# Kernel optimization log

Measured on AMD Instinct MI355X. Metric: run time of the kernel, lower is better.

## Reference

```python
import jax, jax.numpy as jnp
import numpy as np

# ---- config (matches init_kwargs + VMamba/MambaIR SS2D defaults) ----
B, LEN, C, H, W = 2, 3, 64, 64, 64
N_STATE = 16           # d_state
D_INNER = 2 * C        # expand=2
DT_RANK = C // 16      # ceil(d_model/16)
K = 4                  # 4 scan directions
EPS = 1e-5


def _ln_last(x, g, b):
    m = x.mean(-1, keepdims=True)
    v = x.var(-1, keepdims=True)
    return (x - m) * jax.lax.rsqrt(v + EPS) * g + b


def _instance_ln(x):
    # kalman.utils.layer_norm: normalize each sample over (C,H,W), no affine
    m = x.mean(axis=(1, 2, 3), keepdims=True)
    v = x.var(axis=(1, 2, 3), keepdims=True)
    return (x - m) * jax.lax.rsqrt(v + EPS)


def _gn(x, g, b):
    # GroupNorm with num_groups=1 on NCHW
    m = x.mean(axis=(1, 2, 3), keepdims=True)
    v = x.var(axis=(1, 2, 3), keepdims=True)
    return (x - m) * jax.lax.rsqrt(v + EPS) * g[None, :, None, None] + b[None, :, None, None]


def _conv2d(x, w, b, groups=1):
    y = jax.lax.conv_general_dilated(x, w, (1, 1), 'SAME',
            dimension_numbers=('NCHW', 'OIHW', 'NCHW'), feature_group_count=groups)
    return y + b[None, :, None, None]


def _selective_scan(xs, dts, Bs, Cs, A, Ds, dt_bias):
    # xs, dts: (Bt,K,D,L); Bs, Cs: (Bt,K,N,L); A: (K,D,N); Ds, dt_bias: (K,D)
    delta = jax.nn.softplus(dts + dt_bias[None, :, :, None])
    u_t = jnp.moveaxis(xs, -1, 0)      # (L,Bt,K,D)
    d_t = jnp.moveaxis(delta, -1, 0)
    B_t = jnp.moveaxis(Bs, -1, 0)      # (L,Bt,K,N)
    C_t = jnp.moveaxis(Cs, -1, 0)
    h0 = jnp.zeros((xs.shape[0], K, xs.shape[2], A.shape[-1]), xs.dtype)

    def step(h, inp):
        u, d, Bv, Cv = inp
        dA = jnp.exp(d[..., None] * A)                                  # (Bt,K,D,N)
        h = dA * h + d[..., None] * Bv[:, :, None, :] * u[..., None]
        y = jnp.einsum('bkdn,bkn->bkd', h, Cv)
        return h, y

    _, ys = jax.lax.scan(step, h0, (u_t, d_t, B_t, C_t))
    ys = jnp.moveaxis(ys, 0, -1)                                        # (Bt,K,D,L)
    return ys + xs * Ds[None, :, :, None]


def _ss2d(x, in_proj_w, dwconv_w, dwconv_b, x_proj_w, dt_proj_w, dt_proj_b,
          A_logs, Ds, out_norm_g, out_norm_b, out_proj_w):
    Bt, Hh, Ww, Cc = x.shape
    L = Hh * Ww
    xz = x @ in_proj_w.T                               # (Bt,H,W,2*Di)
    xx, z = jnp.split(xz, 2, axis=-1)
    xx = jnp.transpose(xx, (0, 3, 1, 2))               # (Bt,Di,H,W)
    xx = jax.nn.silu(_conv2d(xx, dwconv_w, dwconv_b, groups=D_INNER))
    hw = xx.reshape(Bt, D_INNER, L)
    wh = jnp.transpose(xx, (0, 1, 3, 2)).reshape(Bt, D_INNER, L)
    xs = jnp.stack([hw, wh, hw[..., ::-1], wh[..., ::-1]], axis=1)      # (Bt,4,Di,L)
    x_dbl = jnp.einsum('bkdl,kcd->bkcl', xs, x_proj_w)
    dts = jnp.einsum('bkrl,kdr->bkdl', x_dbl[:, :, :DT_RANK], dt_proj_w)
    Bs = x_dbl[:, :, DT_RANK:DT_RANK + N_STATE]
    Cs = x_dbl[:, :, DT_RANK + N_STATE:]
    A = -jnp.exp(A_logs)                               # (K,Di,N)
    out_y = _selective_scan(xs, dts, Bs, Cs, A, Ds, dt_proj_b)
    inv = out_y[:, 2:4, :, ::-1]

    def wh2hw(y):
        return jnp.transpose(y.reshape(Bt, D_INNER, Ww, Hh), (0, 1, 3, 2)).reshape(Bt, D_INNER, L)

    y = out_y[:, 0] + inv[:, 0] + wh2hw(out_y[:, 1]) + wh2hw(inv[:, 1])
    y = jnp.transpose(y.reshape(Bt, D_INNER, Hh, Ww), (0, 2, 3, 1))
    y = _ln_last(y, out_norm_g, out_norm_b)
    y = y * jax.nn.silu(z)
    return y @ out_proj_w.T


def setup_inputs() -> dict:
    key = jax.random.key(0)
    ks = jax.random.split(key, 16)
    rn = lambda k, s, sc=0.05: jax.random.normal(k, s, jnp.float32) * sc
    inp = {}
    inp['image_sequence'] = jax.random.normal(ks[0], (B, LEN, C, H, W), jnp.float32)
    inp['difficult_zone'] = jax.random.normal(ks[1], (B, C, H, W), jnp.float32)
    inp['sigma'] = jax.random.uniform(ks[2], (B, C, H, W), jnp.float32)
    inp['gn1_g'] = jnp.ones((3 * C,)); inp['gn1_b'] = jnp.zeros((3 * C,))
    inp['conv1_w'] = rn(ks[3], (C, 3 * C, 3, 3)); inp['conv1_b'] = jnp.zeros((C,))
    inp['gn2_g'] = jnp.ones((C,)); inp['gn2_b'] = jnp.zeros((C,))
    inp['conv2_w'] = rn(ks[4], (C, C, 3, 3)); inp['conv2_b'] = jnp.zeros((C,))
    inp['skip_w'] = rn(ks[5], (C, 3 * C, 1, 1)); inp['skip_b'] = jnp.zeros((C,))
    inp['ln1_g'] = jnp.ones((C,)); inp['ln1_b'] = jnp.zeros((C,))
    inp['ln2_g'] = jnp.ones((C,)); inp['ln2_b'] = jnp.zeros((C,))
    inp['in_proj_w'] = rn(ks[6], (2 * D_INNER, C))
    inp['dwconv_w'] = rn(ks[7], (D_INNER, 1, 3, 3)); inp['dwconv_b'] = jnp.zeros((D_INNER,))
    inp['x_proj_w'] = rn(ks[8], (K, DT_RANK + 2 * N_STATE, D_INNER))
    inp['dt_proj_w'] = rn(ks[9], (K, D_INNER, DT_RANK), 0.2)
    inp['dt_proj_b'] = rn(ks[10], (K, D_INNER), 0.1)
    inp['A_logs'] = jnp.log(jnp.broadcast_to(jnp.arange(1, N_STATE + 1, dtype=jnp.float32), (K, D_INNER, N_STATE)))
    inp['Ds'] = jnp.ones((K, D_INNER))
    inp['out_norm_g'] = jnp.ones((D_INNER,)); inp['out_norm_b'] = jnp.zeros((D_INNER,))
    inp['out_proj_w'] = rn(ks[11], (C, D_INNER))
    inp['fc1_w'] = rn(ks[12], (C, C)); inp['fc1_b'] = jnp.zeros((C,))
    inp['fc2_w'] = rn(ks[13], (C, C)); inp['fc2_b'] = jnp.zeros((C,))
    return inp


def reference(image_sequence, difficult_zone, sigma,
              gn1_g, gn1_b, conv1_w, conv1_b, gn2_g, gn2_b, conv2_w, conv2_b, skip_w, skip_b,
              ln1_g, ln1_b, ln2_g, ln2_b,
              in_proj_w, dwconv_w, dwconv_b, x_proj_w, dt_proj_w, dt_proj_b,
              A_logs, Ds, out_norm_g, out_norm_b, out_proj_w,
              fc1_w, fc1_b, fc2_w, fc2_b):
    Bsz, Lf, Cc, Hh, Ww = image_sequence.shape
    # per-frame layer_norm; frames are independent so fold them into batch
    img = _instance_ln(image_sequence.reshape(Bsz * Lf, Cc, Hh, Ww)).reshape(Bsz, Lf, Cc, Hh, Ww)
    dz = jnp.broadcast_to(difficult_zone[:, None], (Bsz, Lf, Cc, Hh, Ww))
    sg = jnp.broadcast_to(sigma[:, None], (Bsz, Lf, Cc, Hh, Ww))
    x = jnp.concatenate([dz, img, sg], axis=2).reshape(Bsz * Lf, 3 * Cc, Hh, Ww)
    # ConvolutionalResBlock (GN -> SiLU -> conv, x2, + 1x1 skip)
    h = _conv2d(jax.nn.silu(_gn(x, gn1_g, gn1_b)), conv1_w, conv1_b)
    h = _conv2d(jax.nn.silu(_gn(h, gn2_g, gn2_b)), conv2_w, conv2_b)
    x = h + _conv2d(x, skip_w, skip_b)
    # VSSBlock (pre-norm): x + SS2D(LN(x)); x + Mlp(LN(x))
    x = jnp.transpose(x, (0, 2, 3, 1))                 # NHWC
    x = x + _ss2d(_ln_last(x, ln1_g, ln1_b), in_proj_w, dwconv_w, dwconv_b,
                  x_proj_w, dt_proj_w, dt_proj_b, A_logs, Ds,
                  out_norm_g, out_norm_b, out_proj_w)
    xm = _ln_last(x, ln2_g, ln2_b)
    x = x + (jax.nn.gelu(xm @ fc1_w.T + fc1_b) @ fc2_w.T + fc2_b)
    x = jnp.transpose(x, (0, 3, 1, 2)).reshape(Bsz, Lf, Cc, Hh, Ww)
    return x
```

## Files before the change

kernel.cpp:

```cpp
#include <hip/hip_runtime.h>
#include <hip/hip_bf16.h>

typedef unsigned short ushortT;
typedef short short8v __attribute__((ext_vector_type(8)));
typedef short short4v __attribute__((ext_vector_type(4)));
typedef float float4v __attribute__((ext_vector_type(4)));

#define NBL 6
#define NC 64
#define NC3 192
#define NHW 4096
#define NK 4
#define NL 4096
#define NCH 128
#define SCLEN 32
#define NSTATE 49152
#define NSAMP 262144

static const size_t F_XCAT  = 0;
static const size_t F_ACT1  = 4718592;
static const size_t F_H1    = 9437184;
static const size_t F_ACT2  = 11010048;
static const size_t F_H2    = 12582912;
static const size_t F_XRES  = 14155776;
static const size_t F_XXIN  = 15728640;
static const size_t F_Z     = 18874368;
static const size_t F_XXC   = 22020096;
static const size_t F_XDBL  = 25165824;
static const size_t F_YS    = 28704768;
static const size_t F_WTS   = 41287680;
static const size_t F_X1    = 44433408;
static const size_t F_X2    = 46006272;
static const size_t F_STATS = 47579136;
static const size_t F_TOTAL = 47579184;

__device__ __forceinline__ float wred64(float v) {
#pragma unroll
  for (int m = 32; m; m >>= 1) v += __shfl_xor(v, m, 64);
  return v;
}

__device__ __forceinline__ float silu(float v) {
  return v / (1.f + __expf(-v));
}

__device__ __forceinline__ ushortT f2bf(float f) {
  unsigned int u = __builtin_bit_cast(unsigned int, f);
  unsigned int r = (u + 0x7FFFu + ((u >> 16) & 1u)) >> 16;
  return (ushortT)r;
}

__device__ __forceinline__ float bf2f(ushortT u) {
  return __builtin_bit_cast(float, (unsigned int)u << 16);
}

__device__ __forceinline__ int map_pos(int k, int l) {
  if (k == 0) return l;
  if (k == 1) return ((l & 63) << 6) | (l >> 6);
  if (k == 2) return 4095 - l;
  int lp = 4095 - l;
  return ((lp & 63) << 6) | (lp >> 6);
}

__device__ __forceinline__ float softplus_fast(float a) {
  float t = exp2f(a * 1.44269504f);
  float r = 0.69314718f * __log2f(1.f + t);
  return (a > 20.f) ? a : r;
}

__device__ __forceinline__ void pow_tree(float E1, float4v& e0, float4v& e1,
                                         float4v& e2, float4v& e3) {
  float E2 = E1 * E1, E3 = E2 * E1, E4 = E2 * E2;
  float E5 = E4 * E1, E6 = E4 * E2, E7 = E4 * E3, E8 = E4 * E4;
  e0[0] = E1; e0[1] = E2; e0[2] = E3; e0[3] = E4;
  e1[0] = E5; e1[1] = E6; e1[2] = E7; e1[3] = E8;
  e2[0] = E8 * E1; e2[1] = E8 * E2; e2[2] = E8 * E3; e2[3] = E8 * E4;
  e3[0] = E8 * E5; e3[1] = E8 * E6; e3[2] = E8 * E7; e3[3] = E8 * E8;
}

__global__ __launch_bounds__(256) void prep_kernel(const float* __restrict__ skw,
                                                   const float* __restrict__ ipw,
                                                   const float* __restrict__ opw,
                                                   const float* __restrict__ f1w,
                                                   const float* __restrict__ f2w,
                                                   const float* __restrict__ c1w,
                                                   const float* __restrict__ c2w,
                                                   const float* __restrict__ Alog,
                                                   float* __restrict__ wt_sk,
                                                   float* __restrict__ wt_ip,
                                                   float* __restrict__ wt_op,
                                                   float* __restrict__ wt_f1,
                                                   float* __restrict__ wt_f2,
                                                   ushortT* __restrict__ wb1,
                                                   ushortT* __restrict__ wb2,
                                                   float* __restrict__ aParam) {
  int bi = blockIdx.x;
  int t = threadIdx.x;
  if (bi < 48) {
    int id = bi * 256 + t;
    int c = id / 64, o = id % 64;
    wt_sk[id] = skw[o * 192 + c];
  } else if (bi < 112) {
    int id = (bi - 48) * 256 + t;
    int c = id / 256, o = id % 256;
    wt_ip[id] = ipw[o * 64 + c];
  } else if (bi < 144) {
    int id = (bi - 112) * 256 + t;
    int c = id / 64, o = id % 64;
    wt_op[id] = opw[o * 128 + c];
  } else if (bi < 160) {
    int id = (bi - 144) * 256 + t;
    int c = id / 64, o = id % 64;
    wt_f1[id] = f1w[o * 64 + c];
  } else if (bi < 176) {
    int id = (bi - 160) * 256 + t;
    int c = id / 64, o = id % 64;
    wt_f2[id] = f2w[o * 64 + c];
  } else if (bi < 608) {
    int id = (bi - 176) * 256 + t;
    int j = id & 7, lane = (id >> 3) & 63, nt = (id >> 9) & 3;
    int rest = id >> 11;
    int kt = rest % 6, tap = rest / 6;
    int oc = nt * 16 + (lane & 15);
    int ic = kt * 32 + ((lane >> 4) << 3) + j;
    int r = tap / 3, s = tap % 3;
    wb1[id] = f2bf(c1w[(((size_t)oc * 192 + ic) * 3 + r) * 3 + s]);
  } else if (bi < 752) {
    int id = (bi - 608) * 256 + t;
    int j = id & 7, lane = (id >> 3) & 63, nt = (id >> 9) & 3;
    int rest = id >> 11;
    int kt = rest % 2, tap = rest / 2;
    int oc = nt * 16 + (lane & 15);
    int ic = kt * 32 + ((lane >> 4) << 3) + j;
    int r = tap / 3, s = tap % 3;
    wb2[id] = f2bf(c2w[(((size_t)oc * 64 + ic) * 3 + r) * 3 + s]);
  } else {
    int kd = (bi - 752) * 256 + t;
    const float* ar = Alog + (size_t)kd * 16;
    float a1v = -__expf(ar[0]) * 1.44269504f;
    bool geom = true;
#pragma unroll
    for (int n = 1; n < 16; ++n) {
      float an = -__expf(ar[n]) * 1.44269504f;
      geom = geom && (fabsf(an - (float)(n + 1) * a1v) <= 1e-3f * fabsf((float)(n + 1) * a1v) + 1e-6f);
    }
    aParam[kd] = a1v;
    aParam[512 + kd] = geom ? 1.f : 0.f;
  }
}

__global__ __launch_bounds__(256) void stats1_all_kernel(const float* __restrict__ img,
                                                         const float* __restrict__ dz,
                                                         const float* __restrict__ sg,
                                                         double* __restrict__ part) {
  int bi = blockIdx.x;
  int s = bi >> 5, j = bi & 31;
  const float* srcb = (s < 6) ? (img + (size_t)s * NSAMP)
                   : (s < 8) ? (dz + (size_t)(s - 6) * NSAMP)
                             : (sg + (size_t)(s - 8) * NSAMP);
  int slice = NSAMP >> 5;
  const float4* p = (const float4*)(srcb + (size_t)j * slice);
  int n4 = slice >> 2;
  double dsum = 0.0, dsq = 0.0;
  for (int i = threadIdx.x; i < n4; i += 256) {
    float4 v = p[i];
    dsum += (double)((v.x + v.y) + (v.z + v.w));
    dsq += (double)v.x * v.x + (double)v.y * v.y + (double)v.z * v.z + (double)v.w * v.w;
  }
  __shared__ double s1[256], s2[256];
  s1[threadIdx.x] = dsum; s2[threadIdx.x] = dsq;
  __syncthreads();
  for (int off = 128; off; off >>= 1) {
    if (threadIdx.x < off) { s1[threadIdx.x] += s1[threadIdx.x + off]; s2[threadIdx.x] += s2[threadIdx.x + off]; }
    __syncthreads();
  }
  if (threadIdx.x == 0) { part[2 * bi] = s1[0]; part[2 * bi + 1] = s2[0]; }
}

__global__ __launch_bounds__(256) void stats1_kernel(const float* __restrict__ in, int n,
                                                     double* __restrict__ part) {
  int bi = blockIdx.x;
  int s = bi >> 5, j = bi & 31;
  int slice = n >> 5;
  const float4* p = (const float4*)(in + (size_t)s * n + (size_t)j * slice);
  int n4 = slice >> 2;
  double dsum = 0.0, dsq = 0.0;
  for (int i = threadIdx.x; i < n4; i += 256) {
    float4 v = p[i];
    dsum += (double)((v.x + v.y) + (v.z + v.w));
    dsq += (double)v.x * v.x + (double)v.y * v.y + (double)v.z * v.z + (double)v.w * v.w;
  }
  __shared__ double s1[256], s2[256];
  s1[threadIdx.x] = dsum; s2[threadIdx.x] = dsq;
  __syncthreads();
  for (int off = 128; off; off >>= 1) {
    if (threadIdx.x < off) { s1[threadIdx.x] += s1[threadIdx.x + off]; s2[threadIdx.x] += s2[threadIdx.x + off]; }
    __syncthreads();
  }
  if (threadIdx.x == 0) { part[2 * bi] = s1[0]; part[2 * bi + 1] = s2[0]; }
}

__global__ __launch_bounds__(64) void stats2_kernel(const double* __restrict__ part, int n,
                                                    float* __restrict__ mean_out,
                                                    float* __restrict__ rstd_out) {
  int s = blockIdx.x;
  int lane = threadIdx.x;
  double sum = 0.0, sq = 0.0;
  if (lane < 32) { sum = part[2 * (s * 32 + lane)]; sq = part[2 * (s * 32 + lane) + 1]; }
#pragma unroll
  for (int m = 16; m; m >>= 1) { sum += __shfl_xor(sum, m, 64); sq += __shfl_xor(sq, m, 64); }
  if (lane == 0) {
    double mean = sum / n;
    double var = sq / n - mean * mean;
    mean_out[s] = (float)mean;
    rstd_out[s] = (float)(1.0 / sqrt(var + 1e-5));
  }
}

__global__ __launch_bounds__(64) void stats2_comb_kernel(const double* __restrict__ part,
                                                         float* __restrict__ stats) {
  int s = blockIdx.x;
  int lane = threadIdx.x;
  if (s < 6) {
    double sum = 0.0, sq = 0.0;
    if (lane < 32) { sum = part[2 * (s * 32 + lane)]; sq = part[2 * (s * 32 + lane) + 1]; }
#pragma unroll
    for (int m = 16; m; m >>= 1) { sum += __shfl_xor(sum, m, 64); sq += __shfl_xor(sq, m, 64); }
    if (lane == 0) {
      double mean = sum / NSAMP;
      double var = sq / NSAMP - mean * mean;
      stats[s] = (float)mean;
      stats[8 + s] = (float)(1.0 / sqrt(var + 1e-5));
    }
    return;
  }
  if (lane == 0) {
    double sums[10], sqs[10];
    for (int q = 0; q < 10; ++q) {
      double a = 0.0, b2 = 0.0;
      for (int j = 0; j < 32; ++j) { a += part[2 * (q * 32 + j)]; b2 += part[2 * (q * 32 + j) + 1]; }
      sums[q] = a; sqs[q] = b2;
    }
    const double N = (double)NSAMP;
    for (int bl = 0; bl < 6; ++bl) {
      int b = bl / 3;
      double mi = sums[bl] / N;
      double vi = sqs[bl] / N - mi * mi;
      double ssq_norm = N * (vi / (vi + 1e-5));
      double sum_cat = sums[6 + b] + sums[8 + b];
      double ssq_cat = sqs[6 + b] + ssq_norm + sqs[8 + b];
      double mean = sum_cat / (3.0 * N);
      double var = ssq_cat / (3.0 * N) - mean * mean;
      stats[16 + bl] = (float)mean;
      stats[24 + bl] = (float)(1.0 / sqrt(var + 1e-5));
    }
  }
}

__global__ __launch_bounds__(256) void gnsilu_cat_kernel(const float* __restrict__ img,
                                                         const float* __restrict__ dz,
                                                         const float* __restrict__ sg,
                                                         const float* __restrict__ g,
                                                         const float* __restrict__ b,
                                                         const float* __restrict__ stats,
                                                         ushortT* __restrict__ outb) {
  int bi = blockIdx.x;
  int bl = bi >> 6, h = bi & 63;
  int bb = bl / 3;
  __shared__ ushortT tile[NC3][66];
  float mi = stats[bl], rsi = stats[8 + bl];
  float mc = stats[16 + bl], rsc = stats[24 + bl];
  int t = threadIdx.x;
  for (int idx = t; idx < NC3 * 64; idx += 256) {
    int ch = idx >> 6, w = idx & 63;
    int hw = (h << 6) + w;
    float v;
    if (ch < 64) v = dz[((size_t)bb * NC + ch) * NHW + hw];
    else if (ch < 128) v = (img[((size_t)bl * NC + (ch - 64)) * NHW + hw] - mi) * rsi;
    else v = sg[((size_t)bb * NC + (ch - 128)) * NHW + hw];
    v = (v - mc) * rsc * g[ch] + b[ch];
    tile[ch][w] = f2bf(silu(v));
  }
  __syncthreads();
  constexpr int C8 = NC3 / 8;
  for (int idx = t; idx < 64 * C8; idx += 256) {
    int w = idx / C8, c8 = idx % C8;
    short8v v;
#pragma unroll
    for (int j = 0; j < 8; ++j) v[j] = (short)tile[c8 * 8 + j][w];
    *(short8v*)&outb[(size_t)(bl * 4096 + h * 64 + w) * NC3 + c8 * 8] = v;
  }
}

__global__ __launch_bounds__(256) void gnsilu_t_kernel(const float* __restrict__ in,
                                                       const float* __restrict__ g,
                                                       const float* __restrict__ b,
                                                       const float* __restrict__ stats,
                                                       ushortT* __restrict__ outb) {
  int bi = blockIdx.x;
  int bl = bi >> 6, h = bi & 63;
  __shared__ ushortT tile[NC][66];
  float m = stats[bl], rs = stats[8 + bl];
  int t = threadIdx.x;
  for (int idx = t; idx < NC * 64; idx += 256) {
    int ch = idx >> 6, w = idx & 63;
    float v = in[(((size_t)bl * NC + ch) << 12) + (h << 6) + w];
    v = (v - m) * rs * g[ch] + b[ch];
    tile[ch][w] = f2bf(silu(v));
  }
  __syncthreads();
  constexpr int C8 = NC / 8;
  for (int idx = t; idx < 64 * C8; idx += 256) {
    int w = idx / C8, c8 = idx % C8;
    short8v v;
#pragma unroll
    for (int j = 0; j < 8; ++j) v[j] = (short)tile[c8 * 8 + j][w];
    *(short8v*)&outb[(size_t)(bl * 4096 + h * 64 + w) * NC + c8 * 8] = v;
  }
}

template <int CIN>
__global__ __launch_bounds__(256) void conv_mfma_kernel(const ushortT* __restrict__ actb,
                                                        const ushortT* __restrict__ wb,
                                                        const float* __restrict__ bias,
                                                        float* __restrict__ out) {
  constexpr int KT = CIN / 32;
  constexpr int STRIDE = CIN + 8;
  constexpr int C8 = CIN / 8;
  int bi = blockIdx.x;
  int nh = bi & 1;
  int h = (bi >> 1) & 63;
  int bl = bi >> 7;
  int t = threadIdx.x;
  int wv = t >> 6, lane = t & 63;
  __shared__ ushortT lds[66 * STRIDE];
  float4v acc0 = {0.f, 0.f, 0.f, 0.f};
  float4v acc1 = {0.f, 0.f, 0.f, 0.f};
  int lrow = lane & 15;
  int lk = (lane >> 4) << 3;
  for (int dy = 0; dy < 3; ++dy) {
    int hh = h + dy - 1;
    bool valid = (hh >= 0) && (hh < 64);
    int hc = valid ? hh : 0;
    if (dy) __syncthreads();
    const ushortT* src = actb + (size_t)(bl * 4096 + hc * 64) * CIN;
    for (int idx = t; idx < 64 * C8; idx += 256) {
      int w = idx / C8, c8 = idx % C8;
      short8v v = {0, 0, 0, 0, 0, 0, 0, 0};
      if (valid) v = *(const short8v*)&src[(size_t)w * CIN + c8 * 8];
      *(short8v*)&lds[(w + 1) * STRIDE + c8 * 8] = v;
    }
    if (t < 2 * C8) {
      int which = t / C8, c8 = t % C8;
      short8v z = {0, 0, 0, 0, 0, 0, 0, 0};
      *(short8v*)&lds[(which ? 65 : 0) * STRIDE + c8 * 8] = z;
    }
    __syncthreads();
    for (int dx = 0; dx < 3; ++dx) {
      int tap = dy * 3 + dx;
      int wl = (wv << 4) + lrow + dx;
#pragma unroll
      for (int kt = 0; kt < KT; ++kt) {
        short8v a = *(const short8v*)&lds[wl * STRIDE + kt * 32 + lk];
        const ushortT* wp = wb + ((size_t)(((tap * KT + kt) * 4 + (nh << 1)) * 64 + lane) << 3);
        short8v b0 = *(const short8v*)&wp[0];
        short8v b1 = *(const short8v*)&wp[512];
        acc0 = __builtin_amdgcn_mfma_f32_16x16x32_bf16(a, b0, acc0, 0, 0, 0);
        acc1 = __builtin_amdgcn_mfma_f32_16x16x32_bf16(a, b1, acc1, 0, 0, 0);
      }
    }
  }
  int oc0 = (nh << 5) + lrow;
  int oc1 = oc0 + 16;
  int w0 = (wv << 4) + ((lane >> 4) << 2);
  float bv0 = bias[oc0], bv1 = bias[oc1];
  float4 o0 = make_float4(acc0[0] + bv0, acc0[1] + bv0, acc0[2] + bv0, acc0[3] + bv0);
  float4 o1 = make_float4(acc1[0] + bv1, acc1[1] + bv1, acc1[2] + bv1, acc1[3] + bv1);
  *(float4*)&out[(((size_t)bl * 64 + oc0) << 12) + (h << 6) + w0] = o0;
  *(float4*)&out[(((size_t)bl * 64 + oc1) << 12) + (h << 6) + w0] = o1;
}

__global__ __launch_bounds__(256) void skip_kernel(const float* __restrict__ img,
                                                   const float* __restrict__ dz,
                                                   const float* __restrict__ sg,
                                                   const float* __restrict__ stats,
                                                   const float* __restrict__ h2,
                                                   const float* __restrict__ skwt,
                                                   const float* __restrict__ skb,
                                                   float* __restrict__ xres) {
  int bi = blockIdx.x;
  int bl = bi >> 6, h = bi & 63;
  int bb = bl / 3;
  int t = threadIdx.x;
  int oc = t & 63, w0 = (t >> 6) << 4;
  float mi = stats[bl], rsi = stats[8 + bl];
  __shared__ float lds[64][64];
  float acc[16];
#pragma unroll
  for (int i = 0; i < 16; ++i) acc[i] = 0.f;
  for (int cc = 0; cc < 3; ++cc) {
    __syncthreads();
    for (int idx = t; idx < 4096; idx += 256) {
      int ch = idx >> 6, w = idx & 63;
      int hw = (h << 6) + w;
      float v;
      if (cc == 0) v = dz[((size_t)bb * NC + ch) * NHW + hw];
      else if (cc == 1) v = (img[((size_t)bl * NC + ch) * NHW + hw] - mi) * rsi;
      else v = sg[((size_t)bb * NC + ch) * NHW + hw];
      lds[ch][w] = v;
    }
    __syncthreads();
    for (int ch = 0; ch < 64; ++ch) {
      float wv = skwt[((cc << 6) + ch) * 64 + oc];
#pragma unroll
      for (int i = 0; i < 16; ++i) acc[i] += wv * lds[ch][w0 + i];
    }
  }
  float bv = skb[oc];
  int p0 = (h << 6) + w0;
#pragma unroll
  for (int i = 0; i < 16; ++i) {
    float hv = h2[(((size_t)bl * 64 + oc) << 12) + p0 + i];
    xres[((size_t)bl * NHW + p0 + i) * 64 + oc] = acc[i] + bv + hv;
  }
}

__global__ __launch_bounds__(256) void inproj_kernel(const float* __restrict__ xres,
                                                     const float* __restrict__ g,
                                                     const float* __restrict__ b,
                                                     const float* __restrict__ wt,
                                                     float* __restrict__ xxin,
                                                     float* __restrict__ z) {
  int wv = threadIdx.x >> 6, lane = threadIdx.x & 63;
  size_t pi0 = (size_t)blockIdx.x << 4;
  __shared__ float xb[64][16];
  float gv = g[lane], bv = b[lane];
#pragma unroll
  for (int j = 0; j < 4; ++j) {
    int p = (wv << 2) + j;
    float x = xres[(pi0 + p) * 64 + lane];
    float s = wred64(x);
    float s2 = wred64(x * x);
    float m = s * (1.f / 64), var = s2 * (1.f / 64) - m * m;
    float rstd = rsqrtf(var + 1e-5f);
    xb[lane][p] = (x - m) * rstd * gv + bv;
  }
  __syncthreads();
  int oc = (wv << 6) + lane;
  float4v a0 = {0.f, 0.f, 0.f, 0.f}, a1 = a0, a2 = a0, a3 = a0;
  for (int c = 0; c < 64; ++c) {
    float w = wt[(c << 8) + oc];
    const float4v* xr = (const float4v*)&xb[c][0];
    a0 += w * xr[0];
    a1 += w * xr[1];
    a2 += w * xr[2];
    a3 += w * xr[3];
  }
  float acc[16];
  *(float4v*)&acc[0] = a0;
  *(float4v*)&acc[4] = a1;
  *(float4v*)&acc[8] = a2;
  *(float4v*)&acc[12] = a3;
  float* dst = (oc < 128) ? xxin : z;
  int oco = (oc < 128) ? oc : (oc - 128);
#pragma unroll
  for (int p = 0; p < 16; ++p) dst[((pi0 + p) << 7) + oco] = acc[p];
}

__global__ __launch_bounds__(256) void dwconv_kernel(const float* __restrict__ xx,
                                                     const float* __restrict__ w,
                                                     const float* __restrict__ b,
                                                     float* __restrict__ out) {
  size_t gid = (size_t)blockIdx.x * 256 + threadIdx.x;
  int d = gid & 127;
  size_t pi = gid >> 7;
  int p = (int)(pi & 4095);
  int bl = (int)(pi >> 12);
  int h = p >> 6, wq = p & 63;
  float acc = b[d];
  const float* wr = w + d * 9;
#pragma unroll
  for (int dy = -1; dy <= 1; ++dy) {
    int hh = h + dy;
    if (hh < 0 || hh >= 64) continue;
#pragma unroll
    for (int dx = -1; dx <= 1; ++dx) {
      int ww = wq + dx;
      if (ww < 0 || ww >= 64) continue;
      acc += wr[(dy + 1) * 3 + (dx + 1)] * xx[(((size_t)bl << 12) + (hh << 6) + ww) * 128 + d];
    }
  }
  out[pi * 128 + d] = silu(acc);
}

__global__ __launch_bounds__(256) void xdbl_kernel(const float* __restrict__ xxc,
                                                   const float* __restrict__ xpw,
                                                   float* __restrict__ xdbl) {
  int bi = blockIdx.x;
  int lt = bi & 63;
  int korder = (bi >> 6) & 1;
  int bl = bi >> 7;
  int lbase = lt << 6;
  __shared__ float xs[64 * 128];
  int t = threadIdx.x;
#pragma unroll
  for (int it = 0; it < 8; ++it) {
    int idx = it * 256 + t;
    int i = idx >> 5, d4 = idx & 31;
    int l = lbase + i;
    int pos = korder ? (((l & 63) << 6) | (l >> 6)) : l;
    float4 v = *(const float4*)&xxc[((size_t)bl * NHW + pos) * 128 + (d4 << 2)];
    int slot = d4 ^ (i & 7);
    *(float4*)&xs[i * 128 + (slot << 2)] = v;
  }
  __syncthreads();
  int wv = __builtin_amdgcn_readfirstlane(t >> 6);
  int lane = t & 63;
  int k_w = korder + ((wv >= 2) ? 2 : 0);
  int c0 = (wv & 1) * 18;
  float acc[18];
#pragma unroll
  for (int j = 0; j < 18; ++j) acc[j] = 0.f;
  const float* wbase = xpw + (size_t)(k_w * 36 + c0) * 128;
  for (int d4 = 0; d4 < 32; ++d4) {
    int slot = d4 ^ (lane & 7);
    float4 x4 = *(const float4*)&xs[lane * 128 + (slot << 2)];
#pragma unroll
    for (int j = 0; j < 18; ++j) {
      float4 w4 = *(const float4*)&wbase[j * 128 + (d4 << 2)];
      acc[j] += w4.x * x4.x + w4.y * x4.y + w4.z * x4.z + w4.w * x4.w;
    }
  }
  int lout = (k_w < 2) ? (lbase + lane) : (4095 - lbase - lane);
  size_t obase = ((size_t)(bl * 4 + k_w) * 36 + c0) * (size_t)NL + lout;
#pragma unroll
  for (int j = 0; j < 18; ++j)
    xdbl[obase + (size_t)j * NL] = acc[j];
}

__global__ __launch_bounds__(256) void scan_pass1_kernel(const float* __restrict__ xdbl,
                                                         const float* __restrict__ xxc,
                                                         const float* __restrict__ dtw,
                                                         const float* __restrict__ dtb,
                                                         const float* __restrict__ Alog,
                                                         const float* __restrict__ aParam,
                                                         float* __restrict__ chunkSdt,
                                                         ushortT* __restrict__ chunkH16) {
  int bi = blockIdx.x;
  int half = threadIdx.x >> 7;
  int d = threadIdx.x & 127;
  int chunk = ((bi & 63) << 1) + half;
  int bk = bi >> 6;
  int k = bk & 3, bl = bk >> 2;
  float4 wv = *(const float4*)(dtw + (size_t)(((k << 7) + d) << 2));
  float bias = dtb[(k << 7) + d];
  int kd = (k << 7) + d;
  float a1v = aParam[kd];
  bool geom = aParam[512 + kd] > 0.5f;
  __shared__ float xd[2][SCLEN][20];
  int l0 = chunk << 5;
  for (int idx = d; idx < 20 * SCLEN; idx += 128) {
    int c = idx >> 5, li = idx & 31;
    xd[half][li][c] = xdbl[((size_t)bk * 36 + c) * (size_t)NL + l0 + li];
  }
  __syncthreads();
  const float* uB = xxc + ((size_t)bl << 19) + d;
  float4v h0 = {0.f, 0.f, 0.f, 0.f}, h1 = h0, h2 = h0, h3 = h0;
  float sdt = 0.f;
  float u_nxt = uB[(size_t)map_pos(k, l0) << 7];
  if (geom) {
#pragma unroll 2
    for (int li = 0; li < SCLEN; ++li) {
      float u = u_nxt;
      int nl = (li < SCLEN - 1) ? (li + 1) : (SCLEN - 1);
      u_nxt = uB[(size_t)map_pos(k, l0 + nl) << 7];
      const float4v* row = (const float4v*)&xd[half][li][0];
      float4v q0 = row[0];
      float accq = bias + wv.x * q0[0] + wv.y * q0[1] + wv.z * q0[2] + wv.w * q0[3];
      float dt = softplus_fast(accq);
      float dtu = dt * u;
      sdt += dt;
      float4v b0 = row[1], b1 = row[2], b2 = row[3], b3 = row[4];
      float4v e0, e1, e2, e3;
      pow_tree(exp2f(a1v * dt), e0, e1, e2, e3);
      h0 = e0 * h0 + dtu * b0;
      h1 = e1 * h1 + dtu * b1;
      h2 = e2 * h2 + dtu * b2;
      h3 = e3 * h3 + dtu * b3;
    }
  } else {
    const float* ar = Alog + (size_t)kd * 16;
    float4v a0v, a1q, a2q, a3q;
#pragma unroll
    for (int j = 0; j < 4; ++j) {
      a0v[j] = -__expf(ar[j]) * 1.44269504f;
      a1q[j] = -__expf(ar[4 + j]) * 1.44269504f;
      a2q[j] = -__expf(ar[8 + j]) * 1.44269504f;
      a3q[j] = -__expf(ar[12 + j]) * 1.44269504f;
    }
    for (int li = 0; li < SCLEN; ++li) {
      float u = u_nxt;
      int nl = (li < SCLEN - 1) ? (li + 1) : (SCLEN - 1);
      u_nxt = uB[(size_t)map_pos(k, l0 + nl) << 7];
      const float4v* row = (const float4v*)&xd[half][li][0];
      float4v q0 = row[0];
      float accq = bias + wv.x * q0[0] + wv.y * q0[1] + wv.z * q0[2] + wv.w * q0[3];
      float dt = softplus_fast(accq);
      float dtu = dt * u;
      sdt += dt;
      float4v b0 = row[1], b1 = row[2], b2 = row[3], b3 = row[4];
      float4v e0, e1, e2, e3;
#pragma unroll
      for (int j = 0; j < 4; ++j) {
        e0[j] = exp2f(a0v[j] * dt);
        e1[j] = exp2f(a1q[j] * dt);
        e2[j] = exp2f(a2q[j] * dt);
        e3[j] = exp2f(a3q[j] * dt);
      }
      h0 = e0 * h0 + dtu * b0;
      h1 = e1 * h1 + dtu * b1;
      h2 = e2 * h2 + dtu * b2;
      h3 = e3 * h3 + dtu * b3;
    }
  }
  size_t base = (size_t)chunk * NSTATE + (((size_t)bk << 7) + (size_t)d) * 16;
  chunkSdt[(size_t)chunk * 3072 + (bk << 7) + d] = sdt;
  short8v s0, s1;
#pragma unroll
  for (int j = 0; j < 4; ++j) {
    s0[j] = (short)f2bf(h0[j]);
    s0[4 + j] = (short)f2bf(h1[j]);
    s1[j] = (short)f2bf(h2[j]);
    s1[4 + j] = (short)f2bf(h3[j]);
  }
  *(short8v*)&chunkH16[base + 0] = s0;
  *(short8v*)&chunkH16[base + 8] = s1;
}

__global__ __launch_bounds__(256) void scan_pass2_kernel(const float* __restrict__ chunkSdt,
                                                         const ushortT* __restrict__ chunkH16,
                                                         const float* __restrict__ Alog,
                                                         ushortT* __restrict__ chunkHS16) {
  size_t s4 = ((size_t)blockIdx.x * 256 + threadIdx.x) * 4;
  int kd = (int)(s4 >> 4);
  int abase = (int)(s4 & 8191);
  float4v an;
#pragma unroll
  for (int j = 0; j < 4; ++j) an[j] = -__expf(Alog[abase + j]) * 1.44269504f;
  float4v h = {0.f, 0.f, 0.f, 0.f};
  for (int j = 0; j < NCH; ++j) {
    size_t idx = (size_t)j * NSTATE + s4;
    short4v hs;
#pragma unroll
    for (int q = 0; q < 4; ++q) hs[q] = (short)f2bf(h[q]);
    *(short4v*)&chunkHS16[idx] = hs;
    float sdt = chunkSdt[(size_t)j * 3072 + kd];
    short4v hv = *(const short4v*)&chunkH16[idx];
#pragma unroll
    for (int q = 0; q < 4; ++q)
      h[q] = exp2f(an[q] * sdt) * h[q] + bf2f((ushortT)hv[q]);
  }
}

__global__ __launch_bounds__(256) void scan_pass3_kernel(const float* __restrict__ xdbl,
                                                         const float* __restrict__ xxc,
                                                         const float* __restrict__ dtw,
                                                         const float* __restrict__ dtb,
                                                         const float* __restrict__ Alog,
                                                         const float* __restrict__ aParam,
                                                         const ushortT* __restrict__ chunkHS16,
                                                         ushortT* __restrict__ ys16) {
  int bi = blockIdx.x;
  int half = threadIdx.x >> 7;
  int d = threadIdx.x & 127;
  int chunk = ((bi & 63) << 1) + half;
  int bk = bi >> 6;
  int k = bk & 3, bl = bk >> 2;
  float4 wv = *(const float4*)(dtw + (size_t)(((k << 7) + d) << 2));
  float bias = dtb[(k << 7) + d];
  int kd = (k << 7) + d;
  float a1v = aParam[kd];
  bool geom = aParam[512 + kd] > 0.5f;
  __shared__ float xd[2][SCLEN][40];
  int l0 = chunk << 5;
  for (int idx = d; idx < 36 * SCLEN; idx += 128) {
    int c = idx >> 5, li = idx & 31;
    xd[half][li][c] = xdbl[((size_t)bk * 36 + c) * (size_t)NL + l0 + li];
  }
  __syncthreads();
  const float* uB = xxc + ((size_t)bl << 19) + d;
  ushortT* yB = ys16 + ((size_t)bk << 19) + d;
  size_t base = (size_t)chunk * NSTATE + (((size_t)bk << 7) + (size_t)d) * 16;
  float4v h0, h1, h2, h3;
  {
    short8v s0 = *(const short8v*)&chunkHS16[base + 0];
    short8v s1 = *(const short8v*)&chunkHS16[base + 8];
#pragma unroll
    for (int j = 0; j < 4; ++j) {
      h0[j] = bf2f((ushortT)s0[j]);
      h1[j] = bf2f((ushortT)s0[4 + j]);
      h2[j] = bf2f((ushortT)s1[j]);
      h3[j] = bf2f((ushortT)s1[4 + j]);
    }
  }
  float u_nxt = uB[(size_t)map_pos(k, l0) << 7];
  if (geom) {
#pragma unroll 2
    for (int li = 0; li < SCLEN; ++li) {
      float u = u_nxt;
      int nl = (li < SCLEN - 1) ? (li + 1) : (SCLEN - 1);
      u_nxt = uB[(size_t)map_pos(k, l0 + nl) << 7];
      const float4v* row = (const float4v*)&xd[half][li][0];
      float4v q0 = row[0];
      float accq = bias + wv.x * q0[0] + wv.y * q0[1] + wv.z * q0[2] + wv.w * q0[3];
      float dt = softplus_fast(accq);
      float dtu = dt * u;
      float4v b0 = row[1], b1 = row[2], b2 = row[3], b3 = row[4];
      float4v c0 = row[5], c1 = row[6], c2 = row[7], c3 = row[8];
      float4v e0, e1, e2, e3;
      pow_tree(exp2f(a1v * dt), e0, e1, e2, e3);
      h0 = e0 * h0 + dtu * b0;
      h1 = e1 * h1 + dtu * b1;
      h2 = e2 * h2 + dtu * b2;
      h3 = e3 * h3 + dtu * b3;
      float4v sy = h0 * c0;
      sy += h1 * c1;
      sy += h2 * c2;
      sy += h3 * c3;
      yB[(size_t)(l0 + li) << 7] = f2bf((sy[0] + sy[1]) + (sy[2] + sy[3]));
    }
  } else {
    const float* ar = Alog + (size_t)kd * 16;
    float4v a0v, a1q, a2q, a3q;
#pragma unroll
    for (int j = 0; j < 4; ++j) {
      a0v[j] = -__expf(ar[j]) * 1.44269504f;
      a1q[j] = -__expf(ar[4 + j]) * 1.44269504f;
      a2q[j] = -__expf(ar[8 + j]) * 1.44269504f;
      a3q[j] = -__expf(ar[12 + j]) * 1.44269504f;
    }
    for (int li = 0; li < SCLEN; ++li) {
      float u = u_nxt;
      int nl = (li < SCLEN - 1) ? (li + 1) : (SCLEN - 1);
      u_nxt = uB[(size_t)map_pos(k, l0 + nl) << 7];
      const float4v* row = (const float4v*)&xd[half][li][0];
      float4v q0 = row[0];
      float accq = bias + wv.x * q0[0] + wv.y * q0[1] + wv.z * q0[2] + wv.w * q0[3];
      float dt = softplus_fast(accq);
      float dtu = dt * u;
      float4v b0 = row[1], b1 = row[2], b2 = row[3], b3 = row[4];
      float4v c0 = row[5], c1 = row[6], c2 = row[7], c3 = row[8];
      float4v e0, e1, e2, e3;
#pragma unroll
      for (int j = 0; j < 4; ++j) {
        e0[j] = exp2f(a0v[j] * dt);
        e1[j] = exp2f(a1q[j] * dt);
        e2[j] = exp2f(a2q[j] * dt);
        e3[j] = exp2f(a3q[j] * dt);
      }
      h0 = e0 * h0 + dtu * b0;
      h1 = e1 * h1 + dtu * b1;
      h2 = e2 * h2 + dtu * b2;
      h3 = e3 * h3 + dtu * b3;
      float4v sy = h0 * c0;
      sy += h1 * c1;
      sy += h2 * c2;
      sy += h3 * c3;
      yB[(size_t)(l0 + li) << 7] = f2bf((sy[0] + sy[1]) + (sy[2] + sy[3]));
    }
  }
}

__global__ __launch_bounds__(256) void outproj_kernel(const ushortT* __restrict__ ys16,
                                                      const float* __restrict__ xxc,
                                                      const float* __restrict__ Ds,
                                                      const float* __restrict__ z,
                                                      const float* __restrict__ ong,
                                                      const float* __restrict__ onb,
                                                      const float* __restrict__ opwt,
                                                      const float* __restrict__ xres,
                                                      float* __restrict__ x1) {
  int wv = threadIdx.x >> 6, lane = threadIdx.x & 63;
  size_t pi0 = (size_t)blockIdx.x << 4;
  __shared__ float gb[128][16];
  float og0 = ong[lane], ob0 = onb[lane];
  float og1 = ong[64 + lane], ob1 = onb[64 + lane];
  float ds0 = Ds[lane] + Ds[128 + lane] + Ds[256 + lane] + Ds[384 + lane];
  float ds1 = Ds[64 + lane] + Ds[192 + lane] + Ds[320 + lane] + Ds[448 + lane];
#pragma unroll
  for (int j = 0; j < 4; ++j) {
    int p = (wv << 2) + j;
    size_t pp = pi0 + p;
    int bl = (int)(pp >> 12);
    int pg = (int)(pp & 4095);
    int h = pg >> 6, w = pg & 63;
    int l1 = (w << 6) | h;
    size_t base = ((size_t)bl * 4) << 12;
    size_t i0 = (base + pg) << 7;
    size_t i1 = (base + 4096 + l1) << 7;
    size_t i2 = (base + 2 * 4096 + (4095 - pg)) << 7;
    size_t i3 = (base + 3 * 4096 + (4095 - l1)) << 7;
    float xx0 = xxc[(pp << 7) + lane], xx1 = xxc[(pp << 7) + 64 + lane];
    float y0 = bf2f(ys16[i0 + lane]) + bf2f(ys16[i1 + lane]) + bf2f(ys16[i2 + lane]) +
               bf2f(ys16[i3 + lane]) + xx0 * ds0;
    float y1 = bf2f(ys16[i0 + 64 + lane]) + bf2f(ys16[i1 + 64 + lane]) +
               bf2f(ys16[i2 + 64 + lane]) + bf2f(ys16[i3 + 64 + lane]) + xx1 * ds1;
    float s = wred64(y0 + y1);
    float s2 = wred64(y0 * y0 + y1 * y1);
    float m = s * (1.f / 128), var = s2 * (1.f / 128) - m * m;
    float rstd = rsqrtf(var + 1e-5f);
    float z0 = z[(pp << 7) + lane], z1 = z[(pp << 7) + 64 + lane];
    gb[lane][p] = ((y0 - m) * rstd * og0 + ob0) * silu(z0);
    gb[64 + lane][p] = ((y1 - m) * rstd * og1 + ob1) * silu(z1);
  }
  __syncthreads();
  int p0 = wv << 2;
  float4v acc = {0.f, 0.f, 0.f, 0.f};
  for (int c = 0; c < 128; ++c) {
    float w = opwt[(c << 6) + lane];
    acc += w * (*(const float4v*)&gb[c][p0]);
  }
  float accs[4];
  *(float4v*)&accs[0] = acc;
#pragma unroll
  for (int j = 0; j < 4; ++j) {
    size_t pp = pi0 + p0 + j;
    x1[pp * 64 + lane] = xres[pp * 64 + lane] + accs[j];
  }
}

__global__ __launch_bounds__(256) void mlp_kernel(const float* __restrict__ x1,
                                                  const float* __restrict__ g2,
                                                  const float* __restrict__ b2,
                                                  const float* __restrict__ w1t,
                                                  const float* __restrict__ bb1,
                                                  const float* __restrict__ w2t,
                                                  const float* __restrict__ bb2,
                                                  float* __restrict__ out) {
  int wv = threadIdx.x >> 6, lane = threadIdx.x & 63;
  size_t pi0 = (size_t)blockIdx.x << 4;
  __shared__ float xb[64][16], tb[64][16];
  __shared__ float ot[64][17];
  float gv = g2[lane], bv = b2[lane];
  float xsave[4];
#pragma unroll
  for (int j = 0; j < 4; ++j) {
    int p = (wv << 2) + j;
    float xv = x1[(pi0 + p) * 64 + lane];
    xsave[j] = xv;
    float s = wred64(xv), s2 = wred64(xv * xv);
    float m = s * (1.f / 64), var = s2 * (1.f / 64) - m * m;
    float rstd = rsqrtf(var + 1e-5f);
    xb[lane][p] = (xv - m) * rstd * gv + bv;
  }
  __syncthreads();
  int p0 = wv << 2;
  float bb1v = bb1[lane];
  float4v acc = {bb1v, bb1v, bb1v, bb1v};
  for (int c = 0; c < 64; ++c) {
    float w = w1t[(c << 6) + lane];
    acc += w * (*(const float4v*)&xb[c][p0]);
  }
  float us[4];
  *(float4v*)&us[0] = acc;
#pragma unroll
  for (int j = 0; j < 4; ++j) {
    float u = us[j];
    float tt = tanhf(0.7978845608028654f * (u + 0.044715f * u * u * u));
    tb[lane][p0 + j] = 0.5f * u * (1.f + tt);
  }
  __syncthreads();
  float bb2v = bb2[lane];
  float4v acc2 = {bb2v, bb2v, bb2v, bb2v};
  for (int c = 0; c < 64; ++c) {
    float w = w2t[(c << 6) + lane];
    acc2 += w * (*(const float4v*)&tb[c][p0]);
  }
  float o2[4];
  *(float4v*)&o2[0] = acc2;
#pragma unroll
  for (int j = 0; j < 4; ++j)
    ot[lane][p0 + j] = xsave[j] + o2[j];
  __syncthreads();
  int bl = (int)(pi0 >> 12);
  int pg0 = (int)(pi0 & 4095);
  int t = threadIdx.x;
  int c = t >> 2, q = t & 3;
  float4 v = make_float4(ot[c][(q << 2) + 0], ot[c][(q << 2) + 1],
                         ot[c][(q << 2) + 2], ot[c][(q << 2) + 3]);
  *(float4*)&out[(((size_t)bl * 64 + c) << 12) + pg0 + (q << 2)] = v;
}

extern "C" void kernel_launch(void* const* d_in, const int* in_sizes, int n_in,
                              void* d_out, int out_size, void* d_ws, size_t ws_size,
                              hipStream_t stream) {
  const float* img  = (const float*)d_in[0];
  const float* dz   = (const float*)d_in[1];
  const float* sg   = (const float*)d_in[2];
  const float* gn1g = (const float*)d_in[3];
  const float* gn1b = (const float*)d_in[4];
  const float* c1w  = (const float*)d_in[5];
  const float* c1b  = (const float*)d_in[6];
  const float* gn2g = (const float*)d_in[7];
  const float* gn2b = (const float*)d_in[8];
  const float* c2w  = (const float*)d_in[9];
  const float* c2b  = (const float*)d_in[10];
  const float* skw  = (const float*)d_in[11];
  const float* skb  = (const float*)d_in[12];
  const float* ln1g = (const float*)d_in[13];
  const float* ln1b = (const float*)d_in[14];
  const float* ln2g = (const float*)d_in[15];
  const float* ln2b = (const float*)d_in[16];
  const float* ipw  = (const float*)d_in[17];
  const float* dww  = (const float*)d_in[18];
  const float* dwb  = (const float*)d_in[19];
  const float* xpw  = (const float*)d_in[20];
  const float* dtw  = (const float*)d_in[21];
  const float* dtb  = (const float*)d_in[22];
  const float* Alog = (const float*)d_in[23];
  const float* Dsp  = (const float*)d_in[24];
  const float* ong  = (const float*)d_in[25];
  const float* onb  = (const float*)d_in[26];
  const float* opw  = (const float*)d_in[27];
  const float* f1w  = (const float*)d_in[28];
  const float* f1b  = (const float*)d_in[29];
  const float* f2w  = (const float*)d_in[30];
  const float* f2b  = (const float*)d_in[31];

  float* out = (float*)d_out;
  float* ws = (float*)d_ws;
  if (ws_size < F_TOTAL * sizeof(float)) return;

  float* h1    = ws + F_H1;
  float* h2    = ws + F_H2;
  float* xres  = ws + F_XRES;
  float* xxin  = ws + F_XXIN;
  float* zbuf  = ws + F_Z;
  float* xxc   = ws + F_XXC;
  float* xdbl  = ws + F_XDBL;
  float* x1    = ws + F_X1;
  float* stats = ws + F_STATS;
  ushortT* act1b = (ushortT*)(ws + F_ACT1);
  ushortT* act2b = (ushortT*)(ws + F_ACT2);
  double* part  = (double*)(ws + F_X2);
  float* wt_sk = ws + F_WTS;
  float* wt_ip = ws + F_WTS + 16384;
  float* wt_op = ws + F_WTS + 32768;
  float* wt_f1 = ws + F_WTS + 40960;
  float* wt_f2 = ws + F_WTS + 45056;
  ushortT* wb1 = (ushortT*)(ws + F_WTS + 49152);
  ushortT* wb2 = wb1 + 110592;
  float* aParam = ws + F_WTS + 49152 + 73728 + 1024;
  ushortT* ys16     = (ushortT*)(ws + F_YS);
  ushortT* chunkH16 = (ushortT*)(ws + F_YS + 6291456);
  float*   chunkSdt = ws + F_YS + 6291456 + 3145728;
  ushortT* chunkHS16 = (ushortT*)(ws + F_XCAT);

  prep_kernel<<<754, 256, 0, stream>>>(skw, ipw, opw, f1w, f2w, c1w, c2w, Alog,
                                       wt_sk, wt_ip, wt_op, wt_f1, wt_f2, wb1, wb2, aParam);
  stats1_all_kernel<<<320, 256, 0, stream>>>(img, dz, sg, part);
  stats2_comb_kernel<<<7, 64, 0, stream>>>(part, stats);
  gnsilu_cat_kernel<<<NBL * 64, 256, 0, stream>>>(img, dz, sg, gn1g, gn1b, stats, act1b);
  conv_mfma_kernel<NC3><<<NBL * 64 * 2, 256, 0, stream>>>(act1b, wb1, c1b, h1);
  stats1_kernel<<<NBL * 32, 256, 0, stream>>>(h1, NC * NHW, part);
  stats2_kernel<<<NBL, 64, 0, stream>>>(part, NC * NHW, stats + 32, stats + 40);
  gnsilu_t_kernel<<<NBL * 64, 256, 0, stream>>>(h1, gn2g, gn2b, stats + 32, act2b);
  conv_mfma_kernel<NC><<<NBL * 64 * 2, 256, 0, stream>>>(act2b, wb2, c2b, h2);
  skip_kernel<<<NBL * 64, 256, 0, stream>>>(img, dz, sg, stats, h2, wt_sk, skb, xres);
  inproj_kernel<<<1536, 256, 0, stream>>>(xres, ln1g, ln1b, wt_ip, xxin, zbuf);
  dwconv_kernel<<<12288, 256, 0, stream>>>(xxin, dww, dwb, xxc);
  xdbl_kernel<<<NBL * 2 * 64, 256, 0, stream>>>(xxc, xpw, xdbl);
  scan_pass1_kernel<<<24 * 64, 256, 0, stream>>>(xdbl, xxc, dtw, dtb, Alog, aParam, chunkSdt, chunkH16);
  scan_pass2_kernel<<<48, 256, 0, stream>>>(chunkSdt, chunkH16, Alog, chunkHS16);
  scan_pass3_kernel<<<24 * 64, 256, 0, stream>>>(xdbl, xxc, dtw, dtb, Alog, aParam, chunkHS16, ys16);
  outproj_kernel<<<1536, 256, 0, stream>>>(ys16, xxc, Dsp, zbuf, ong, onb, wt_op, xres, x1);
  mlp_kernel<<<1536, 256, 0, stream>>>(x1, ln2g, ln2b, wt_f1, f1b, wt_f2, f2b, out);
}
```

Baseline: 328.3 us.

## Store in-proj and dwconv activations as bf16 and split scan blocks to 128 threads

The x branch of the in-projection and the depthwise-conv output are now stored as bf16 instead of fp32. Every consumer (dwconv, xdbl, scan passes 1 and 3, outproj) converts on load, which halves the memory traffic for these tensors. Scan passes 1 and 3 now launch one 128-thread block per chunk instead of pairing two chunks in a 256-thread block, which may improve scheduling granularity. The cost is lower precision on the scan input u and the D-skip term.

```diff
diff --git a/kernel.cpp b/kernel.cpp
--- a/kernel.cpp
+++ b/kernel.cpp
@@ -429,7 +429,7 @@
                                                      const float* __restrict__ g,
                                                      const float* __restrict__ b,
                                                      const float* __restrict__ wt,
-                                                     float* __restrict__ xxin,
+                                                     ushortT* __restrict__ xxin16,
                                                      float* __restrict__ z) {
   int wv = threadIdx.x >> 6, lane = threadIdx.x & 63;
   size_t pi0 = (size_t)blockIdx.x << 4;
@@ -461,16 +461,20 @@
   *(float4v*)&acc[4] = a1;
   *(float4v*)&acc[8] = a2;
   *(float4v*)&acc[12] = a3;
-  float* dst = (oc < 128) ? xxin : z;
-  int oco = (oc < 128) ? oc : (oc - 128);
-#pragma unroll
-  for (int p = 0; p < 16; ++p) dst[((pi0 + p) << 7) + oco] = acc[p];
-}
-
-__global__ __launch_bounds__(256) void dwconv_kernel(const float* __restrict__ xx,
+  if (oc < 128) {
+#pragma unroll
+    for (int p = 0; p < 16; ++p) xxin16[((pi0 + p) << 7) + oc] = f2bf(acc[p]);
+  } else {
+    int oco = oc - 128;
+#pragma unroll
+    for (int p = 0; p < 16; ++p) z[((pi0 + p) << 7) + oco] = acc[p];
+  }
+}
+
+__global__ __launch_bounds__(256) void dwconv_kernel(const ushortT* __restrict__ xx,
                                                      const float* __restrict__ w,
                                                      const float* __restrict__ b,
-                                                     float* __restrict__ out) {
+                                                     ushortT* __restrict__ out) {
   size_t gid = (size_t)blockIdx.x * 256 + threadIdx.x;
   int d = gid & 127;
   size_t pi = gid >> 7;
@@ -487,13 +491,13 @@
     for (int dx = -1; dx <= 1; ++dx) {
       int ww = wq + dx;
       if (ww < 0 || ww >= 64) continue;
-      acc += wr[(dy + 1) * 3 + (dx + 1)] * xx[(((size_t)bl << 12) + (hh << 6) + ww) * 128 + d];
-    }
-  }
-  out[pi * 128 + d] = silu(acc);
-}
-
-__global__ __launch_bounds__(256) void xdbl_kernel(const float* __restrict__ xxc,
+      acc += wr[(dy + 1) * 3 + (dx + 1)] * bf2f(xx[(((size_t)bl << 12) + (hh << 6) + ww) * 128 + d]);
+    }
+  }
+  out[pi * 128 + d] = f2bf(silu(acc));
+}
+
+__global__ __launch_bounds__(256) void xdbl_kernel(const ushortT* __restrict__ xxc16,
                                                    const float* __restrict__ xpw,
                                                    float* __restrict__ xdbl) {
   int bi = blockIdx.x;
@@ -504,14 +508,19 @@
   __shared__ float xs[64 * 128];
   int t = threadIdx.x;
 #pragma unroll
-  for (int it = 0; it < 8; ++it) {
+  for (int it = 0; it < 4; ++it) {
     int idx = it * 256 + t;
-    int i = idx >> 5, d4 = idx & 31;
+    int i = idx >> 4, d8 = idx & 15;
     int l = lbase + i;
     int pos = korder ? (((l & 63) << 6) | (l >> 6)) : l;
-    float4 v = *(const float4*)&xxc[((size_t)bl * NHW + pos) * 128 + (d4 << 2)];
-    int slot = d4 ^ (i & 7);
-    *(float4*)&xs[i * 128 + (slot << 2)] = v;
+    short8v v8 = *(const short8v*)&xxc16[((size_t)bl * NHW + pos) * 128 + (d8 << 3)];
+    float4 va = make_float4(bf2f((ushortT)v8[0]), bf2f((ushortT)v8[1]),
+                            bf2f((ushortT)v8[2]), bf2f((ushortT)v8[3]));
+    float4 vb = make_float4(bf2f((ushortT)v8[4]), bf2f((ushortT)v8[5]),
+                            bf2f((ushortT)v8[6]), bf2f((ushortT)v8[7]));
+    int d4a = d8 << 1, d4b = d4a + 1;
+    *(float4*)&xs[i * 128 + ((d4a ^ (i & 7)) << 2)] = va;
+    *(float4*)&xs[i * 128 + ((d4b ^ (i & 7)) << 2)] = vb;
   }
   __syncthreads();
   int wv = __builtin_amdgcn_readfirstlane(t >> 6);
@@ -538,8 +547,8 @@
     xdbl[obase + (size_t)j * NL] = acc[j];
 }
 
-__global__ __launch_bounds__(256) void scan_pass1_kernel(const float* __restrict__ xdbl,
-                                                         const float* __restrict__ xxc,
+__global__ __launch_bounds__(128) void scan_pass1_kernel(const float* __restrict__ xdbl,
+                                                         const ushortT* __restrict__ xxc16,
                                                          const float* __restrict__ dtw,
                                                          const float* __restrict__ dtb,
                                                          const float* __restrict__ Alog,
@@ -547,34 +556,33 @@
                                                          float* __restrict__ chunkSdt,
                                                          ushortT* __restrict__ chunkH16) {
   int bi = blockIdx.x;
-  int half = threadIdx.x >> 7;
-  int d = threadIdx.x & 127;
-  int chunk = ((bi & 63) << 1) + half;
-  int bk = bi >> 6;
+  int chunk = bi & (NCH - 1);
+  int bk = bi >> 7;
   int k = bk & 3, bl = bk >> 2;
+  int d = threadIdx.x;
   float4 wv = *(const float4*)(dtw + (size_t)(((k << 7) + d) << 2));
   float bias = dtb[(k << 7) + d];
   int kd = (k << 7) + d;
   float a1v = aParam[kd];
   bool geom = aParam[512 + kd] > 0.5f;
-  __shared__ float xd[2][SCLEN][20];
+  __shared__ float xd[SCLEN][20];
   int l0 = chunk << 5;
-  for (int idx = d; idx < 20 * SCLEN; idx += 128) {
+  for (int idx = threadIdx.x; idx < 20 * SCLEN; idx += 128) {
     int c = idx >> 5, li = idx & 31;
-    xd[half][li][c] = xdbl[((size_t)bk * 36 + c) * (size_t)NL + l0 + li];
-  }
-  __syncthreads();
-  const float* uB = xxc + ((size_t)bl << 19) + d;
+    xd[li][c] = xdbl[((size_t)bk * 36 + c) * (size_t)NL + l0 + li];
+  }
+  __syncthreads();
+  const ushortT* uB = xxc16 + ((size_t)bl << 19) + d;
   float4v h0 = {0.f, 0.f, 0.f, 0.f}, h1 = h0, h2 = h0, h3 = h0;
   float sdt = 0.f;
-  float u_nxt = uB[(size_t)map_pos(k, l0) << 7];
+  float u_nxt = bf2f(uB[(size_t)map_pos(k, l0) << 7]);
   if (geom) {
 #pragma unroll 2
     for (int li = 0; li < SCLEN; ++li) {
       float u = u_nxt;
       int nl = (li < SCLEN - 1) ? (li + 1) : (SCLEN - 1);
-      u_nxt = uB[(size_t)map_pos(k, l0 + nl) << 7];
-      const float4v* row = (const float4v*)&xd[half][li][0];
+      u_nxt = bf2f(uB[(size_t)map_pos(k, l0 + nl) << 7]);
+      const float4v* row = (const float4v*)&xd[li][0];
       float4v q0 = row[0];
       float accq = bias + wv.x * q0[0] + wv.y * q0[1] + wv.z * q0[2] + wv.w * q0[3];
       float dt = softplus_fast(accq);
@@ -601,8 +609,8 @@
     for (int li = 0; li < SCLEN; ++li) {
       float u = u_nxt;
       int nl = (li < SCLEN - 1) ? (li + 1) : (SCLEN - 1);
-      u_nxt = uB[(size_t)map_pos(k, l0 + nl) << 7];
-      const float4v* row = (const float4v*)&xd[half][li][0];
+      u_nxt = bf2f(uB[(size_t)map_pos(k, l0 + nl) << 7]);
+      const float4v* row = (const float4v*)&xd[li][0];
       float4v q0 = row[0];
       float accq = bias + wv.x * q0[0] + wv.y * q0[1] + wv.z * q0[2] + wv.w * q0[3];
       float dt = softplus_fast(accq);
@@ -662,8 +670,8 @@
   }
 }
 
-__global__ __launch_bounds__(256) void scan_pass3_kernel(const float* __restrict__ xdbl,
-                                                         const float* __restrict__ xxc,
+__global__ __launch_bounds__(128) void scan_pass3_kernel(const float* __restrict__ xdbl,
+                                                         const ushortT* __restrict__ xxc16,
                                                          const float* __restrict__ dtw,
                                                          const float* __restrict__ dtb,
                                                          const float* __restrict__ Alog,
@@ -671,24 +679,23 @@
                                                          const ushortT* __restrict__ chunkHS16,
                                                          ushortT* __restrict__ ys16) {
   int bi = blockIdx.x;
-  int half = threadIdx.x >> 7;
-  int d = threadIdx.x & 127;
-  int chunk = ((bi & 63) << 1) + half;
-  int bk = bi >> 6;
+  int chunk = bi & (NCH - 1);
+  int bk = bi >> 7;
   int k = bk & 3, bl = bk >> 2;
+  int d = threadIdx.x;
   float4 wv = *(const float4*)(dtw + (size_t)(((k << 7) + d) << 2));
   float bias = dtb[(k << 7) + d];
   int kd = (k << 7) + d;
   float a1v = aParam[kd];
   bool geom = aParam[512 + kd] > 0.5f;
-  __shared__ float xd[2][SCLEN][40];
+  __shared__ float xd[SCLEN][40];
   int l0 = chunk << 5;
-  for (int idx = d; idx < 36 * SCLEN; idx += 128) {
+  for (int idx = threadIdx.x; idx < 36 * SCLEN; idx += 128) {
     int c = idx >> 5, li = idx & 31;
-    xd[half][li][c] = xdbl[((size_t)bk * 36 + c) * (size_t)NL + l0 + li];
-  }
-  __syncthreads();
-  const float* uB = xxc + ((size_t)bl << 19) + d;
+    xd[li][c] = xdbl[((size_t)bk * 36 + c) * (size_t)NL + l0 + li];
+  }
+  __syncthreads();
+  const ushortT* uB = xxc16 + ((size_t)bl << 19) + d;
   ushortT* yB = ys16 + ((size_t)bk << 19) + d;
   size_t base = (size_t)chunk * NSTATE + (((size_t)bk << 7) + (size_t)d) * 16;
   float4v h0, h1, h2, h3;
@@ -703,14 +710,14 @@
       h3[j] = bf2f((ushortT)s1[4 + j]);
     }
   }
-  float u_nxt = uB[(size_t)map_pos(k, l0) << 7];
+  float u_nxt = bf2f(uB[(size_t)map_pos(k, l0) << 7]);
   if (geom) {
 #pragma unroll 2
     for (int li = 0; li < SCLEN; ++li) {
       float u = u_nxt;
       int nl = (li < SCLEN - 1) ? (li + 1) : (SCLEN - 1);
-      u_nxt = uB[(size_t)map_pos(k, l0 + nl) << 7];
-      const float4v* row = (const float4v*)&xd[half][li][0];
+      u_nxt = bf2f(uB[(size_t)map_pos(k, l0 + nl) << 7]);
+      const float4v* row = (const float4v*)&xd[li][0];
       float4v q0 = row[0];
       float accq = bias + wv.x * q0[0] + wv.y * q0[1] + wv.z * q0[2] + wv.w * q0[3];
       float dt = softplus_fast(accq);
@@ -742,8 +749,8 @@
     for (int li = 0; li < SCLEN; ++li) {
       float u = u_nxt;
       int nl = (li < SCLEN - 1) ? (li + 1) : (SCLEN - 1);
-      u_nxt = uB[(size_t)map_pos(k, l0 + nl) << 7];
-      const float4v* row = (const float4v*)&xd[half][li][0];
+      u_nxt = bf2f(uB[(size_t)map_pos(k, l0 + nl) << 7]);
+      const float4v* row = (const float4v*)&xd[li][0];
       float4v q0 = row[0];
       float accq = bias + wv.x * q0[0] + wv.y * q0[1] + wv.z * q0[2] + wv.w * q0[3];
       float dt = softplus_fast(accq);
@@ -772,7 +779,7 @@
 }
 
 __global__ __launch_bounds__(256) void outproj_kernel(const ushortT* __restrict__ ys16,
-                                                      const float* __restrict__ xxc,
+                                                      const ushortT* __restrict__ xxc16,
                                                       const float* __restrict__ Ds,
                                                       const float* __restrict__ z,
                                                       const float* __restrict__ ong,
@@ -800,7 +807,8 @@
     size_t i1 = (base + 4096 + l1) << 7;
     size_t i2 = (base + 2 * 4096 + (4095 - pg)) << 7;
     size_t i3 = (base + 3 * 4096 + (4095 - l1)) << 7;
-    float xx0 = xxc[(pp << 7) + lane], xx1 = xxc[(pp << 7) + 64 + lane];
+    float xx0 = bf2f(xxc16[(pp << 7) + lane]);
+    float xx1 = bf2f(xxc16[(pp << 7) + 64 + lane]);
     float y0 = bf2f(ys16[i0 + lane]) + bf2f(ys16[i1 + lane]) + bf2f(ys16[i2 + lane]) +
                bf2f(ys16[i3 + lane]) + xx0 * ds0;
     float y1 = bf2f(ys16[i0 + 64 + lane]) + bf2f(ys16[i1 + 64 + lane]) +
@@ -934,14 +942,14 @@
   float* h1    = ws + F_H1;
   float* h2    = ws + F_H2;
   float* xres  = ws + F_XRES;
-  float* xxin  = ws + F_XXIN;
   float* zbuf  = ws + F_Z;
-  float* xxc   = ws + F_XXC;
   float* xdbl  = ws + F_XDBL;
   float* x1    = ws + F_X1;
   float* stats = ws + F_STATS;
   ushortT* act1b = (ushortT*)(ws + F_ACT1);
   ushortT* act2b = (ushortT*)(ws + F_ACT2);
+  ushortT* xxin16 = (ushortT*)(ws + F_XXIN);
+  ushortT* xxc16  = (ushortT*)(ws + F_XXC);
   double* part  = (double*)(ws + F_X2);
   float* wt_sk = ws + F_WTS;
   float* wt_ip = ws + F_WTS + 16384;
@@ -967,12 +975,12 @@
   gnsilu_t_kernel<<<NBL * 64, 256, 0, stream>>>(h1, gn2g, gn2b, stats + 32, act2b);
   conv_mfma_kernel<NC><<<NBL * 64 * 2, 256, 0, stream>>>(act2b, wb2, c2b, h2);
   skip_kernel<<<NBL * 64, 256, 0, stream>>>(img, dz, sg, stats, h2, wt_sk, skb, xres);
-  inproj_kernel<<<1536, 256, 0, stream>>>(xres, ln1g, ln1b, wt_ip, xxin, zbuf);
-  dwconv_kernel<<<12288, 256, 0, stream>>>(xxin, dww, dwb, xxc);
-  xdbl_kernel<<<NBL * 2 * 64, 256, 0, stream>>>(xxc, xpw, xdbl);
-  scan_pass1_kernel<<<24 * 64, 256, 0, stream>>>(xdbl, xxc, dtw, dtb, Alog, aParam, chunkSdt, chunkH16);
+  inproj_kernel<<<1536, 256, 0, stream>>>(xres, ln1g, ln1b, wt_ip, xxin16, zbuf);
+  dwconv_kernel<<<12288, 256, 0, stream>>>(xxin16, dww, dwb, xxc16);
+  xdbl_kernel<<<NBL * 2 * 64, 256, 0, stream>>>(xxc16, xpw, xdbl);
+  scan_pass1_kernel<<<24 * NCH, 128, 0, stream>>>(xdbl, xxc16, dtw, dtb, Alog, aParam, chunkSdt, chunkH16);
   scan_pass2_kernel<<<48, 256, 0, stream>>>(chunkSdt, chunkH16, Alog, chunkHS16);
-  scan_pass3_kernel<<<24 * 64, 256, 0, stream>>>(xdbl, xxc, dtw, dtb, Alog, aParam, chunkHS16, ys16);
-  outproj_kernel<<<1536, 256, 0, stream>>>(ys16, xxc, Dsp, zbuf, ong, onb, wt_op, xres, x1);
+  scan_pass3_kernel<<<24 * NCH, 128, 0, stream>>>(xdbl, xxc16, dtw, dtb, Alog, aParam, chunkHS16, ys16);
+  outproj_kernel<<<1536, 256, 0, stream>>>(ys16, xxc16, Dsp, zbuf, ong, onb, wt_op, xres, x1);
   mlp_kernel<<<1536, 256, 0, stream>>>(x1, ln2g, ln2b, wt_f1, f1b, wt_f2, f2b, out);
 }
```

After: 327.2 us. No clear change (-0.3%).
